# Performance work log

Hardware: AMD Instinct MI355X
Metric: run time of the kernel (lower is better)

## Reference

```python
import jax, jax.numpy as jnp
import numpy as np

BIG = 1e10


def _cylinder_query(radius, hmin, hmax, nsample, xyz, new_xyz, rot):
    # xyz: (B,N,3), new_xyz: (B,P,3), rot: (B,P,3,3) -> idx: (B,P,nsample) int32
    diff = xyz[:, None, :, :] - new_xyz[:, :, None, :]          # (B,P,N,3)
    local = jnp.einsum('bpnc,bpcd->bpnd', diff, rot)            # (B,P,N,3)
    x, y, z = local[..., 0], local[..., 1], local[..., 2]
    r2 = y * y + z * z                                          # (B,P,N)
    in_cyl = (x >= hmin) & (x <= hmax) & (r2 < radius * radius)
    dist = jnp.where(in_cyl, r2, BIG)
    neg_vals, idx = jax.lax.top_k(-dist, nsample)               # smallest dists
    vals = -neg_vals
    valid = vals < 1e9
    first = idx[:, :, 0:1]
    idx = jnp.where(valid, idx, first)                          # (B,P,nsample)
    return idx


def _group(features, idx):
    # features: (B,C,N), idx: (B,P,S) -> (B,C,P,S)
    B, C, N = features.shape
    P, S = idx.shape[1], idx.shape[2]
    ft = jnp.swapaxes(features, 1, 2)                           # (B,N,C)
    flat = idx.reshape(B, P * S)
    out = jnp.take_along_axis(ft, flat[:, :, None], axis=1)     # (B,P*S,C)
    return jnp.transpose(out.reshape(B, P, S, C), (0, 3, 1, 2)) # (B,C,P,S)


def setup_inputs() -> dict:
    key = jax.random.key(0)
    k1, k2, k3, k4 = jax.random.split(key, 4)
    B, N, P, C = 4, 16384, 1024, 64
    xyz = jax.random.uniform(k1, (B, N, 3), dtype=jnp.float32)
    new_xyz = jax.random.uniform(k2, (B, P, 3), dtype=jnp.float32)
    rot = jax.random.normal(k3, (B, P, 3, 3), dtype=jnp.float32)
    features = jax.random.normal(k4, (B, C, N), dtype=jnp.float32)
    return {"radius": 0.3, "hmin": -0.02, "hmax": 0.04, "nsample": 32,
            "xyz": xyz, "new_xyz": new_xyz, "rot": rot, "features": features}


def reference(radius, hmin, hmax, nsample, xyz, new_xyz, rot, features):
    idx = _cylinder_query(radius, hmin, hmax, nsample, xyz, new_xyz, rot)
    xyz_t = jnp.swapaxes(xyz, 1, 2)                             # (B,3,N)
    grouped_xyz = _group(xyz_t, idx)                            # (B,3,P,S)
    grouped_xyz = grouped_xyz - jnp.swapaxes(new_xyz, 1, 2)[..., None]
    # rotate_xyz=True: (B,P,S,3) @ (B,P,3,3)
    g = jnp.transpose(grouped_xyz, (0, 2, 3, 1))
    g = jnp.einsum('bpsc,bpcd->bpsd', g, rot)
    grouped_xyz = jnp.transpose(g, (0, 3, 1, 2))                # (B,3,P,S)
    grouped_features = _group(features, idx)                    # (B,C,P,S)
    return jnp.concatenate([grouped_xyz, grouped_features], axis=1)
```

## Files before the change

### kernel.cpp

```cpp
#include <hip/hip_runtime.h>

#define CAP    4608
#define BIGK   1.0e300
#define IDXINF 0x7fffffff

__device__ __forceinline__ void cmpx(double& k, int& n, int lane, int stride, bool up) {
    double ok = __shfl_xor(k, stride);
    int    on = __shfl_xor(n, stride);
    bool oLess = (ok < k) || (ok == k && on < n);
    bool lower = (lane & stride) == 0;
    bool takeOther = lower ? (up ? oLess : !oLess) : (up ? !oLess : oLess);
    if (takeOther) { k = ok; n = on; }
}

__device__ __forceinline__ void wave_sort64(double& k, int& n, int lane, bool asc) {
    #pragma unroll
    for (int size = 2; size < 64; size <<= 1) {
        bool up = asc ? ((lane & size) == 0) : ((lane & size) != 0);
        #pragma unroll
        for (int stride = size >> 1; stride > 0; stride >>= 1)
            cmpx(k, n, lane, stride, up);
    }
    #pragma unroll
    for (int stride = 32; stride > 0; stride >>= 1)
        cmpx(k, n, lane, stride, asc);
}

__global__ __launch_bounds__(256) void select_kernel(
    const float* __restrict__ radius_p,
    const float* __restrict__ hmin_p,
    const float* __restrict__ hmax_p,
    const float* __restrict__ xyz,
    const float* __restrict__ new_xyz,
    const float* __restrict__ rot,
    float* __restrict__ out,
    unsigned short* __restrict__ selw)
{
    const int N = 16384, P = 1024, S = 32, OC = 67;
    const int bp  = blockIdx.x;
    const int b   = bp >> 10;
    const int p   = bp & (P - 1);
    const int tid = threadIdx.x;
    const int lane = tid & 63;
    const int wv   = tid >> 6;

    __shared__ unsigned short cn[CAP];
    __shared__ double wr2[256];
    __shared__ int    wn[256];
    __shared__ int    cnt;
    __shared__ int    cnt2;
    __shared__ int    sel[32];

    if (tid == 0) { cnt = 0; cnt2 = 0; }
    __syncthreads();

    const double radius = (double)radius_p[0];
    const double hmin   = (double)hmin_p[0];
    const double hmax   = (double)hmax_p[0];
    const double rad2   = radius * radius;

    const float* nx = new_xyz + (size_t)bp * 3;
    const double cx = nx[0], cy = nx[1], cz = nx[2];
    const float* rp = rot + (size_t)bp * 9;
    const double r00 = rp[0], r01 = rp[1], r02 = rp[2];
    const double r10 = rp[3], r11 = rp[4], r12 = rp[5];
    const double r20 = rp[6], r21 = rp[7], r22 = rp[8];

    const float cxf = (float)cx, cyf = (float)cy, czf = (float)cz;
    const float r00f = (float)r00, r01f = (float)r01, r02f = (float)r02;
    const float r10f = (float)r10, r11f = (float)r11, r12f = (float)r12;
    const float r20f = (float)r20, r21f = (float)r21, r22f = (float)r22;
    const float hminf = (float)hmin - 5.0e-4f;
    const float hmaxf = (float)hmax + 5.0e-4f;
    const float rad2f = (float)rad2 + 1.0e-3f;

    const float* xb = xyz + (size_t)b * N * 3;

    for (int it = 0; it < 16; ++it) {
        int g = it * 1024 + tid * 4;
        const float4* vp = reinterpret_cast<const float4*>(xb + (size_t)g * 3);
        float4 v0 = vp[0], v1 = vp[1], v2 = vp[2];
        float px[4], py[4], pz[4];
        px[0]=v0.x; py[0]=v0.y; pz[0]=v0.z;
        px[1]=v0.w; py[1]=v1.x; pz[1]=v1.y;
        px[2]=v1.z; py[2]=v1.w; pz[2]=v2.x;
        px[3]=v2.y; py[3]=v2.z; pz[3]=v2.w;
        #pragma unroll
        for (int k = 0; k < 4; ++k) {
            float dxf = px[k] - cxf, dyf = py[k] - cyf, dzf = pz[k] - czf;
            float xf  = fmaf(dxf, r00f, fmaf(dyf, r10f, dzf * r20f));
            float yf  = fmaf(dxf, r01f, fmaf(dyf, r11f, dzf * r21f));
            float zf  = fmaf(dxf, r02f, fmaf(dyf, r12f, dzf * r22f));
            float r2f = fmaf(yf, yf, zf * zf);
            if (xf >= hminf && xf <= hmaxf && r2f < rad2f) {
                int slot = atomicAdd(&cnt, 1);
                if (slot < CAP) cn[slot] = (unsigned short)(g + k);
            }
        }
    }
    __syncthreads();

    const int Mloose = min(cnt, CAP);

    double rk = BIGK; int rn = IDXINF;
    int msum = 0;
    const int nch = (Mloose + 63) >> 6;
    for (int ch = wv; ch < nch; ch += 4) {
        int j = (ch << 6) + lane;
        double ck = BIGK; int cnn = IDXINF;
        bool ok = false;
        if (j < Mloose) {
            int n = cn[j];
            double dx = (double)xb[n * 3 + 0] - cx;
            double dy = (double)xb[n * 3 + 1] - cy;
            double dz = (double)xb[n * 3 + 2] - cz;
            double x = dx * r00 + dy * r10 + dz * r20;
            double y = dx * r01 + dy * r11 + dz * r21;
            double z = dx * r02 + dy * r12 + dz * r22;
            double r2 = y * y + z * z;
            if (x >= hmin && x <= hmax && r2 < rad2) { ok = true; ck = r2; cnn = n; }
        }
        msum += __popcll(__ballot(ok));
        wave_sort64(ck, cnn, lane, false);
        if ((ck < rk) || (ck == rk && cnn < rn)) { rk = ck; rn = cnn; }
        #pragma unroll
        for (int stride = 32; stride > 0; stride >>= 1)
            cmpx(rk, rn, lane, stride, true);
    }
    if (lane == 0 && msum > 0) atomicAdd(&cnt2, msum);
    wr2[(wv << 6) + lane] = rk;
    wn [(wv << 6) + lane] = rn;
    __syncthreads();

    if (wv == 0) {
        const int Mtrue = cnt2;
        #pragma unroll
        for (int w = 1; w < 4; ++w) {
            int src = (w << 6) + (63 - lane);
            double ck = wr2[src]; int cnn = wn[src];
            if ((ck < rk) || (ck == rk && cnn < rn)) { rk = ck; rn = cnn; }
            #pragma unroll
            for (int stride = 32; stride > 0; stride >>= 1)
                cmpx(rk, rn, lane, stride, true);
        }
        int nsel  = min(Mtrue, S);
        int first = __shfl(rn, 0);
        int v = (lane < nsel) ? rn : ((nsel > 0) ? first : 0);
        if (lane < S) sel[lane] = v;
    }
    __syncthreads();

    if (tid < S) {
        int n = sel[tid];
        selw[(size_t)bp * S + tid] = (unsigned short)n;
        double dx = (double)xb[n * 3 + 0] - cx;
        double dy = (double)xb[n * 3 + 1] - cy;
        double dz = (double)xb[n * 3 + 2] - cz;
        float x = (float)(dx * r00 + dy * r10 + dz * r20);
        float y = (float)(dx * r01 + dy * r11 + dz * r21);
        float z = (float)(dx * r02 + dy * r12 + dz * r22);
        float* o = out + (((size_t)b * OC + 0) * P + p) * S + tid;
        o[0 * (size_t)P * S] = x;
        o[1 * (size_t)P * S] = y;
        o[2 * (size_t)P * S] = z;
    }
}

__global__ __launch_bounds__(256) void gather_kernel(
    const float* __restrict__ feat,
    const unsigned short* __restrict__ selw,
    float* __restrict__ out)
{
    const int N = 16384, P = 1024, C = 64, S = 32, OC = 67;
    const int bid  = blockIdx.x;
    const int c    = bid & 63;
    const int half = (bid >> 6) & 1;
    const int b    = bid >> 7;
    const int tid  = threadIdx.x;

    __shared__ unsigned short st[512 * 32];

    const uint4* sp = reinterpret_cast<const uint4*>(
        selw + ((size_t)b * P + half * 512) * S);
    uint4* dl = reinterpret_cast<uint4*>(st);
    #pragma unroll
    for (int k = 0; k < 8; ++k)
        dl[k * 256 + tid] = sp[k * 256 + tid];
    __syncthreads();

    const float* fr = feat + ((size_t)b * C + c) * N;
    float* ob = out + (((size_t)b * OC + 3 + c) * P + half * 512) * S;
    #pragma unroll 4
    for (int k = 0; k < 16; ++k) {
        int e4 = (k * 256 + tid) * 4;
        ushort4 ix = *reinterpret_cast<const ushort4*>(&st[e4]);
        float4 v;
        v.x = fr[ix.x]; v.y = fr[ix.y]; v.z = fr[ix.z]; v.w = fr[ix.w];
        *reinterpret_cast<float4*>(&ob[e4]) = v;
    }
}

extern "C" void kernel_launch(void* const* d_in, const int* in_sizes, int n_in,
                              void* d_out, int out_size, void* d_ws, size_t ws_size,
                              hipStream_t stream) {
    const float* radius  = (const float*)d_in[0];
    const float* hmin    = (const float*)d_in[1];
    const float* hmax    = (const float*)d_in[2];
    const float* xyz     = (const float*)d_in[4];
    const float* new_xyz = (const float*)d_in[5];
    const float* rot     = (const float*)d_in[6];
    const float* feat    = (const float*)d_in[7];
    float* out = (float*)d_out;
    unsigned short* selw = (unsigned short*)d_ws;

    hipLaunchKernelGGL(select_kernel, dim3(4096), dim3(256), 0, stream,
                       radius, hmin, hmax, xyz, new_xyz, rot, out, selw);
    hipLaunchKernelGGL(gather_kernel, dim3(512), dim3(256), 0, stream,
                       feat, selw, out);
}
```

Measured before the change: 122.8 us.

## Prefetch xyz tiles in select loop and split gather into quarter blocks with nontemporal stores

```diff
diff --git a/kernel.cpp b/kernel.cpp
--- a/kernel.cpp
+++ b/kernel.cpp
@@ -3,6 +3,8 @@
 #define CAP    4608
 #define BIGK   1.0e300
 #define IDXINF 0x7fffffff
+
+typedef float  natf4 __attribute__((ext_vector_type(4)));
 
 __device__ __forceinline__ void cmpx(double& k, int& n, int lane, int stride, bool up) {
     double ok = __shfl_xor(k, stride);
@@ -75,16 +77,18 @@
     const float rad2f = (float)rad2 + 1.0e-3f;
 
     const float* xb = xyz + (size_t)b * N * 3;
-
+    const float4* vp = reinterpret_cast<const float4*>(xb);
+
+    float4 a0 = vp[tid * 3 + 0], a1 = vp[tid * 3 + 1], a2 = vp[tid * 3 + 2];
     for (int it = 0; it < 16; ++it) {
+        const float4* q = vp + ((it + 1) & 15) * 768 + tid * 3;
+        float4 b0 = q[0], b1 = q[1], b2 = q[2];
         int g = it * 1024 + tid * 4;
-        const float4* vp = reinterpret_cast<const float4*>(xb + (size_t)g * 3);
-        float4 v0 = vp[0], v1 = vp[1], v2 = vp[2];
         float px[4], py[4], pz[4];
-        px[0]=v0.x; py[0]=v0.y; pz[0]=v0.z;
-        px[1]=v0.w; py[1]=v1.x; pz[1]=v1.y;
-        px[2]=v1.z; py[2]=v1.w; pz[2]=v2.x;
-        px[3]=v2.y; py[3]=v2.z; pz[3]=v2.w;
+        px[0]=a0.x; py[0]=a0.y; pz[0]=a0.z;
+        px[1]=a0.w; py[1]=a1.x; pz[1]=a1.y;
+        px[2]=a1.z; py[2]=a1.w; pz[2]=a2.x;
+        px[3]=a2.y; py[3]=a2.z; pz[3]=a2.w;
         #pragma unroll
         for (int k = 0; k < 4; ++k) {
             float dxf = px[k] - cxf, dyf = py[k] - cyf, dzf = pz[k] - czf;
@@ -97,6 +101,7 @@
                 if (slot < CAP) cn[slot] = (unsigned short)(g + k);
             }
         }
+        a0 = b0; a1 = b1; a2 = b2;
     }
     __syncthreads();
 
@@ -172,31 +177,31 @@
     float* __restrict__ out)
 {
     const int N = 16384, P = 1024, C = 64, S = 32, OC = 67;
-    const int bid  = blockIdx.x;
-    const int c    = bid & 63;
-    const int half = (bid >> 6) & 1;
-    const int b    = bid >> 7;
-    const int tid  = threadIdx.x;
-
-    __shared__ unsigned short st[512 * 32];
+    const int bid = blockIdx.x;
+    const int qtr = bid & 7;
+    const int c   = (bid >> 3) & 63;
+    const int b   = bid >> 9;
+    const int tid = threadIdx.x;
+
+    __shared__ unsigned short st[128 * 32];
 
     const uint4* sp = reinterpret_cast<const uint4*>(
-        selw + ((size_t)b * P + half * 512) * S);
+        selw + ((size_t)b * P + qtr * 128) * S);
     uint4* dl = reinterpret_cast<uint4*>(st);
     #pragma unroll
-    for (int k = 0; k < 8; ++k)
+    for (int k = 0; k < 2; ++k)
         dl[k * 256 + tid] = sp[k * 256 + tid];
     __syncthreads();
 
     const float* fr = feat + ((size_t)b * C + c) * N;
-    float* ob = out + (((size_t)b * OC + 3 + c) * P + half * 512) * S;
-    #pragma unroll 4
-    for (int k = 0; k < 16; ++k) {
+    float* ob = out + (((size_t)b * OC + 3 + c) * P + qtr * 128) * S;
+    #pragma unroll
+    for (int k = 0; k < 4; ++k) {
         int e4 = (k * 256 + tid) * 4;
         ushort4 ix = *reinterpret_cast<const ushort4*>(&st[e4]);
-        float4 v;
+        natf4 v;
         v.x = fr[ix.x]; v.y = fr[ix.y]; v.z = fr[ix.z]; v.w = fr[ix.w];
-        *reinterpret_cast<float4*>(&ob[e4]) = v;
+        __builtin_nontemporal_store(v, reinterpret_cast<natf4*>(&ob[e4]));
     }
 }
 
@@ -215,6 +220,6 @@
 
     hipLaunchKernelGGL(select_kernel, dim3(4096), dim3(256), 0, stream,
                        radius, hmin, hmax, xyz, new_xyz, rot, out, selw);
-    hipLaunchKernelGGL(gather_kernel, dim3(512), dim3(256), 0, stream,
+    hipLaunchKernelGGL(gather_kernel, dim3(2048), dim3(256), 0, stream,
                        feat, selw, out);
 }
```

Measured after the change: 124.8 us. About the same (+1.6%).
